# Kernel optimization log

Hardware: AMD Instinct MI355X
Metric: run time of the kernel (lower is better)

The kernel has to match this reference:

```python
import jax, jax.numpy as jnp
import numpy as np
from jax import lax

B, T, L, H, K, NL, NB = 32, 512, 2048, 512, 3, 2, 256
PAD = (K - 1) // 2
EPS = 1e-5


def _predictor_params(key):
    k1, k2 = jax.random.split(key)
    s = 1.0 / np.sqrt(H * K).astype(np.float32)
    return dict(
        conv_w=jax.random.normal(k1, (NL, H, H, K), jnp.float32) * s,
        conv_b=jnp.zeros((NL, H), jnp.float32),
        ln_g=jnp.ones((NL, H), jnp.float32),
        ln_b=jnp.zeros((NL, H), jnp.float32),
        lin_w=jax.random.normal(k2, (H, 1), jnp.float32) * 0.02,
        lin_b=jnp.zeros((1,), jnp.float32),
    )


def setup_inputs():
    key = jax.random.key(0)
    ks = jax.random.split(key, 8)
    inp = {
        'x': jax.random.normal(ks[0], (B, T, H), jnp.float32),
        'src_mask': jnp.zeros((B, T), bool),
        'duration_target': jax.random.randint(ks[1], (B, T), 0, 8, jnp.int32),
        'pitch_target': jax.random.normal(ks[2], (B, T), jnp.float32),
        'energy_target': jax.random.uniform(ks[3], (B, T), jnp.float32),
        'max_len': L,
    }
    for name, k in zip(('dur', 'pit', 'en'), ks[4:7]):
        for p, v in _predictor_params(k).items():
            inp[name + '_' + p] = v
    inp['pitch_bins'] = jnp.linspace(-3.0, 3.0, NB - 1)
    inp['energy_bins'] = jnp.linspace(0.0, 1.0, NB - 1)
    k1, k2 = jax.random.split(ks[7])
    inp['pitch_emb'] = jax.random.normal(k1, (NB, H), jnp.float32) * 0.02
    inp['energy_emb'] = jax.random.normal(k2, (NB, H), jnp.float32) * 0.02
    return inp


def _layer_norm(h, g, b):
    m = jnp.mean(h, -1, keepdims=True)
    v = jnp.var(h, -1, keepdims=True)
    return (h - m) * lax.rsqrt(v + EPS) * g + b


def _predictor(x, cw, cb, lg, lb, lw, lbias, mask):
    # stack of [Conv1d(k=3,same) -> ReLU -> LayerNorm] x NL, then Linear -> 1
    out = x
    for i in range(NL):
        h = lax.conv_general_dilated(out.transpose(0, 2, 1), cw[i], (1,), [(PAD, PAD)],
                                     dimension_numbers=('NCH', 'OIH', 'NCH'))
        h = h.transpose(0, 2, 1) + cb[i]  # [B, T, H]
        out = _layer_norm(jax.nn.relu(h), lg[i], lb[i])
    out = (out @ lw)[..., 0] + lbias[0]  # [B, T]
    return jnp.where(mask, 0.0, out)


def _length_regulate(x, duration, max_len):
    # vectorized equivalent of the per-token expand+concat+pad loop
    csum = jnp.cumsum(duration, axis=1)                     # [B, T]
    frames = jnp.arange(max_len)                            # [L]
    idx = jax.vmap(lambda c: jnp.searchsorted(c, frames, side='right'))(csum)  # [B, L]
    idx = jnp.clip(idx, 0, x.shape[1] - 1)
    out = jnp.take_along_axis(x, idx[:, :, None], axis=1)   # [B, L, H]
    mel_len = jnp.minimum(csum[:, -1], max_len)             # [B]
    out = out * (frames[None, :] < mel_len[:, None])[..., None]
    return out, mel_len


def reference(x, src_mask, duration_target, pitch_target, energy_target, max_len,
              dur_conv_w, dur_conv_b, dur_ln_g, dur_ln_b, dur_lin_w, dur_lin_b,
              pit_conv_w, pit_conv_b, pit_ln_g, pit_ln_b, pit_lin_w, pit_lin_b,
              en_conv_w, en_conv_b, en_ln_g, en_ln_b, en_lin_w, en_lin_b,
              pitch_bins, energy_bins, pitch_emb, energy_emb):
    log_d = _predictor(x, dur_conv_w, dur_conv_b, dur_ln_g, dur_ln_b, dur_lin_w, dur_lin_b, src_mask)
    pitch_pred = _predictor(x, pit_conv_w, pit_conv_b, pit_ln_g, pit_ln_b, pit_lin_w, pit_lin_b, src_mask)
    energy_pred = _predictor(x, en_conv_w, en_conv_b, en_ln_g, en_ln_b, en_lin_w, en_lin_b, src_mask)
    # torch.bucketize(target, bins) (right=False) == searchsorted side='left'
    p_emb = pitch_emb[jnp.searchsorted(pitch_bins, pitch_target, side='left')]
    e_emb = energy_emb[jnp.searchsorted(energy_bins, energy_target, side='left')]
    x2 = x + p_emb + e_emb
    out, mel_len = _length_regulate(x2, duration_target, max_len)
    return (out, pitch_pred, energy_pred, log_d, mel_len)
```

## Files before the change

### kernel.cpp

```cpp
#include <hip/hip_runtime.h>
#include <hip/hip_bf16.h>

#define B_ 32
#define T_ 512
#define TP_ 514
#define L_ 2048
#define H_ 512
#define NRR (B_*T_)
#define KC_ 1536
#define NB_ 256
#define EPS_ 1e-5f
#define XPE ((size_t)B_ * TP_ * H_)

typedef __bf16 bf16;
typedef __bf16 bf16x8 __attribute__((ext_vector_type(8)));
typedef float f32x4 __attribute__((ext_vector_type(4)));

static const size_t WC_BYTES  = (size_t)6 * H_ * KC_ * 2;
static const size_t XP_BYTES  = XPE * 2;
static const size_t Y_BYTES   = (size_t)3 * NRR * H_ * 2;

__device__ __forceinline__ void gload16(const void* g, void* l) {
    __builtin_amdgcn_global_load_lds(
        (const __attribute__((address_space(1))) unsigned int*)g,
        (__attribute__((address_space(3))) unsigned int*)l, 16, 0, 0);
}

__global__ void k_prep_wc(const float* __restrict__ wd, const float* __restrict__ wp,
                          const float* __restrict__ we, bf16* __restrict__ wc) {
    int e = blockIdx.x * 256 + threadIdx.x;
    if (e >= 6 * H_ * KC_) return;
    int m   = e / (H_ * KC_);
    int rem = e % (H_ * KC_);
    int o  = rem / KC_;
    int r2 = rem % KC_;
    int k  = r2 / H_;
    int c  = r2 % H_;
    int p = m >> 1, i = m & 1;
    const float* w = (p == 0) ? wd : (p == 1 ? wp : we);
    float v = w[((size_t)i * H_ * H_ + (size_t)o * H_ + c) * 3 + k];
    wc[e] = (bf16)v;
}

__global__ void k_pad(const float* __restrict__ x, bf16* __restrict__ xp0,
                      bf16* __restrict__ xp1) {
    int wid = threadIdx.x >> 6, lane = threadIdx.x & 63;
    int row = blockIdx.x * 4 + wid;
    int b = row / TP_, tp = row % TP_;
    bf16* d0 = xp0 + (size_t)row * H_ + lane * 8;
    if (tp == 0 || tp == TP_ - 1) {
        bf16x8 z;
#pragma unroll
        for (int i = 0; i < 8; ++i) z[i] = (bf16)0.0f;
        *(bf16x8*)d0 = z;
#pragma unroll
        for (int p = 0; p < 3; ++p)
            *(bf16x8*)(xp1 + p * XPE + (size_t)row * H_ + lane * 8) = z;
    } else {
        const f32x4* p = (const f32x4*)(x + ((size_t)(b * T_ + tp - 1)) * H_ + lane * 8);
        f32x4 u = p[0], v = p[1];
        bf16x8 o;
        o[0] = (bf16)u[0]; o[1] = (bf16)u[1]; o[2] = (bf16)u[2]; o[3] = (bf16)u[3];
        o[4] = (bf16)v[0]; o[5] = (bf16)v[1]; o[6] = (bf16)v[2]; o[7] = (bf16)v[3];
        *(bf16x8*)d0 = o;
    }
}

__global__ void k_scan(const int* __restrict__ dur, int* __restrict__ csum,
                       float* __restrict__ mel_out) {
    int b = blockIdx.x, t = threadIdx.x;
    __shared__ int s[T_];
    s[t] = dur[b * T_ + t];
    __syncthreads();
    for (int off = 1; off < T_; off <<= 1) {
        int v = (t >= off) ? s[t - off] : 0;
        __syncthreads();
        s[t] += v;
        __syncthreads();
    }
    csum[b * T_ + t] = s[t];
    if (t == T_ - 1) mel_out[b] = (float)((s[t] < L_) ? s[t] : L_);
}

__global__ void k_gather(const float* __restrict__ x, const float* __restrict__ pemb,
                         const float* __restrict__ eemb, const float* __restrict__ pt,
                         const float* __restrict__ et, const float* __restrict__ pbins,
                         const float* __restrict__ ebins, const int* __restrict__ csum,
                         float* __restrict__ out) {
    int bi = blockIdx.x;
    int b  = bi >> 9;
    int l0 = (bi & 511) << 2;
    __shared__ int cs[T_];
    __shared__ float pb[NB_ - 1], eb[NB_ - 1];
    cs[threadIdx.x]       = csum[b * T_ + threadIdx.x];
    cs[threadIdx.x + 256] = csum[b * T_ + threadIdx.x + 256];
    if (threadIdx.x < NB_ - 1) {
        pb[threadIdx.x] = pbins[threadIdx.x];
        eb[threadIdx.x] = ebins[threadIdx.x];
    }
    __syncthreads();
    int wid = threadIdx.x >> 6, lane = threadIdx.x & 63;
    int l = l0 + wid;
    int mel = cs[T_ - 1]; if (mel > L_) mel = L_;
    float* op = out + ((size_t)(b * L_ + l)) * H_ + lane * 8;
    if (l >= mel) {
        f32x4 z = {0.f, 0.f, 0.f, 0.f};
        ((f32x4*)op)[0] = z;
        ((f32x4*)op)[1] = z;
        return;
    }
    int lo = 0, hi = T_;
    while (lo < hi) { int mid = (lo + hi) >> 1; if (cs[mid] <= l) lo = mid + 1; else hi = mid; }
    int idx = (lo < T_ - 1) ? lo : (T_ - 1);
    int rr = b * T_ + idx;
    float pv = pt[rr], ev = et[rr];
    int pi, ei;
    { int a = 0, c = NB_ - 1; while (a < c) { int mid = (a + c) >> 1; if (pb[mid] < pv) a = mid + 1; else c = mid; } pi = a; }
    { int a = 0, c = NB_ - 1; while (a < c) { int mid = (a + c) >> 1; if (eb[mid] < ev) a = mid + 1; else c = mid; } ei = a; }
    const f32x4* xp = (const f32x4*)(x    + (size_t)rr * H_ + lane * 8);
    const f32x4* pp = (const f32x4*)(pemb + (size_t)pi * H_ + lane * 8);
    const f32x4* ep = (const f32x4*)(eemb + (size_t)ei * H_ + lane * 8);
    ((f32x4*)op)[0] = xp[0] + pp[0] + ep[0];
    ((f32x4*)op)[1] = xp[1] + pp[1] + ep[1];
}

template<int LAYER>
__global__ __launch_bounds__(512)
void k_gemm(const bf16* __restrict__ Xp, const bf16* __restrict__ Wall,
            const float* __restrict__ cb0, const float* __restrict__ cb1,
            const float* __restrict__ cb2, bf16* __restrict__ Y) {
    __shared__ bf16 lA[128 * 64];
    __shared__ bf16 lB[256 * 64];

    int bid = blockIdx.x;
    int swz = (bid & 7) * 96 + (bid >> 3);
    int rowblk = swz / 6, colblk = swz % 6;
    int p  = colblk >> 1;
    int oB = (colblk & 1) * 256;
    int rowBase = rowblk * 128;

    const bf16* A = (LAYER == 0) ? Xp : (Xp + (size_t)p * XPE);
    const bf16* W = Wall + ((size_t)(2 * p + LAYER) * H_ + oB) * KC_;
    const float* cbp  = (p == 0) ? cb0 : (p == 1 ? cb1 : cb2);
    const float* bias = cbp + LAYER * H_;

    int tid = threadIdx.x;
    int wid = tid >> 6, lane = tid & 63;
    int wr = wid >> 2, wc = wid & 3;
    int lr = lane & 15, kq = lane >> 4;
    int xr = lr & 7;
    int rsub = lane >> 3;
    int csw  = ((lane & 7) ^ rsub) << 3;
    int b = rowBase >> 9, t0 = rowBase & (T_ - 1);

    f32x4 acc[4][4];
#pragma unroll
    for (int m = 0; m < 4; ++m)
#pragma unroll
        for (int n = 0; n < 4; ++n) acc[m][n] = (f32x4){0.f, 0.f, 0.f, 0.f};

    for (int step = 0; step < 24; ++step) {
        int k  = step >> 3;
        int c0 = (step & 7) << 6;
        const bf16* srcA = A + ((size_t)(b * TP_ + t0 + k)) * H_ + c0;
        const bf16* srcB = W + step * 64;
#pragma unroll
        for (int q = 0; q < 2; ++q) {
            int r0 = (wid * 2 + q) * 8;
            gload16(srcA + (size_t)(r0 + rsub) * H_ + csw, lA + r0 * 64);
        }
#pragma unroll
        for (int q = 0; q < 4; ++q) {
            int r0 = (wid * 4 + q) * 8;
            gload16(srcB + (size_t)(r0 + rsub) * KC_ + csw, lB + r0 * 64);
        }
        __syncthreads();
#pragma unroll
        for (int kk = 0; kk < 64; kk += 32) {
            int co = ((((kk >> 3) + kq) ^ xr)) << 3;
            bf16x8 af[4], bfr[4];
#pragma unroll
            for (int m = 0; m < 4; ++m)
                af[m] = *(const bf16x8*)&lA[(wr * 64 + m * 16 + lr) * 64 + co];
#pragma unroll
            for (int n = 0; n < 4; ++n)
                bfr[n] = *(const bf16x8*)&lB[(wc * 64 + n * 16 + lr) * 64 + co];
#pragma unroll
            for (int m = 0; m < 4; ++m)
#pragma unroll
                for (int n = 0; n < 4; ++n)
                    acc[m][n] = __builtin_amdgcn_mfma_f32_16x16x32_bf16(af[m], bfr[n], acc[m][n], 0, 0, 0);
        }
        __syncthreads();
    }

#pragma unroll
    for (int n = 0; n < 4; ++n) {
        int o = oB + wc * 64 + n * 16 + lr;
        float bi = bias[o];
#pragma unroll
        for (int m = 0; m < 4; ++m) {
            int row = rowBase + wr * 64 + m * 16 + 4 * kq;
#pragma unroll
            for (int r = 0; r < 4; ++r)
                Y[((size_t)p * NRR + row + r) * H_ + o] = (bf16)fmaxf(acc[m][n][r] + bi, 0.f);
        }
    }
}

__global__ void k_ln_store(const bf16* __restrict__ Yin,
                           const float* __restrict__ g0, const float* __restrict__ g1,
                           const float* __restrict__ g2,
                           const float* __restrict__ bb0, const float* __restrict__ bb1,
                           const float* __restrict__ bb2, bf16* __restrict__ xp1) {
    int wid = threadIdx.x >> 6, lane = threadIdx.x & 63;
    int rg = blockIdx.x * 4 + wid;
    int p = rg >> 14, r = rg & (NRR - 1);
    const float* g   = (p == 0) ? g0 : (p == 1 ? g1 : g2);
    const float* bta = (p == 0) ? bb0 : (p == 1 ? bb1 : bb2);
    bf16x8 a = *(const bf16x8*)(Yin + ((size_t)p * NRR + r) * H_ + lane * 8);
    float f[8];
#pragma unroll
    for (int i = 0; i < 8; ++i) f[i] = (float)a[i];
    float s1 = 0.f, s2 = 0.f;
#pragma unroll
    for (int i = 0; i < 8; ++i) { s1 += f[i]; s2 += f[i] * f[i]; }
    for (int m = 1; m < 64; m <<= 1) { s1 += __shfl_xor(s1, m); s2 += __shfl_xor(s2, m); }
    float mean = s1 * (1.f / H_);
    float var  = s2 * (1.f / H_) - mean * mean;
    float rs   = rsqrtf(var + EPS_);
    const f32x4* gp = (const f32x4*)g;
    const f32x4* bp = (const f32x4*)bta;
    f32x4 ga = gp[lane * 2], gb = gp[lane * 2 + 1];
    f32x4 ba = bp[lane * 2], bbv = bp[lane * 2 + 1];
    bf16x8 o;
    o[0] = (bf16)((f[0] - mean) * rs * ga[0] + ba[0]);
    o[1] = (bf16)((f[1] - mean) * rs * ga[1] + ba[1]);
    o[2] = (bf16)((f[2] - mean) * rs * ga[2] + ba[2]);
    o[3] = (bf16)((f[3] - mean) * rs * ga[3] + ba[3]);
    o[4] = (bf16)((f[4] - mean) * rs * gb[0] + bbv[0]);
    o[5] = (bf16)((f[5] - mean) * rs * gb[1] + bbv[1]);
    o[6] = (bf16)((f[6] - mean) * rs * gb[2] + bbv[2]);
    o[7] = (bf16)((f[7] - mean) * rs * gb[3] + bbv[3]);
    int bb = r >> 9, t = r & (T_ - 1);
    *(bf16x8*)(xp1 + (size_t)p * XPE + ((size_t)(bb * TP_ + t + 1)) * H_ + lane * 8) = o;
}

__global__ void k_ln_linear(const bf16* __restrict__ Yin,
                            const float* __restrict__ g0, const float* __restrict__ g1,
                            const float* __restrict__ g2,
                            const float* __restrict__ bb0, const float* __restrict__ bb1,
                            const float* __restrict__ bb2,
                            const float* __restrict__ w0p, const float* __restrict__ w1p,
                            const float* __restrict__ w2p,
                            const float* __restrict__ lb0, const float* __restrict__ lb1,
                            const float* __restrict__ lb2,
                            const unsigned char* __restrict__ mask,
                            float* __restrict__ o0, float* __restrict__ o1,
                            float* __restrict__ o2) {
    int wid = threadIdx.x >> 6, lane = threadIdx.x & 63;
    int rg = blockIdx.x * 4 + wid;
    int p = rg >> 14, r = rg & (NRR - 1);
    const float* g   = ((p == 0) ? g0 : (p == 1 ? g1 : g2)) + H_;
    const float* bta = ((p == 0) ? bb0 : (p == 1 ? bb1 : bb2)) + H_;
    const float* lw  = (p == 0) ? w0p : (p == 1 ? w1p : w2p);
    const float* lb  = (p == 0) ? lb0 : (p == 1 ? lb1 : lb2);
    float*       op  = (p == 0) ? o0 : (p == 1 ? o1 : o2);
    bf16x8 a = *(const bf16x8*)(Yin + ((size_t)p * NRR + r) * H_ + lane * 8);
    float f[8];
#pragma unroll
    for (int i = 0; i < 8; ++i) f[i] = (float)a[i];
    float s1 = 0.f, s2 = 0.f;
#pragma unroll
    for (int i = 0; i < 8; ++i) { s1 += f[i]; s2 += f[i] * f[i]; }
    for (int m = 1; m < 64; m <<= 1) { s1 += __shfl_xor(s1, m); s2 += __shfl_xor(s2, m); }
    float mean = s1 * (1.f / H_);
    float var  = s2 * (1.f / H_) - mean * mean;
    float rs   = rsqrtf(var + EPS_);
    const f32x4* gp = (const f32x4*)g;
    const f32x4* bp = (const f32x4*)bta;
    const f32x4* wp = (const f32x4*)lw;
    f32x4 ga = gp[lane * 2], gb = gp[lane * 2 + 1];
    f32x4 ba = bp[lane * 2], bbv = bp[lane * 2 + 1];
    f32x4 wa = wp[lane * 2], wb = wp[lane * 2 + 1];
    float s = ((f[0] - mean) * rs * ga[0] + ba[0]) * wa[0]
            + ((f[1] - mean) * rs * ga[1] + ba[1]) * wa[1]
            + ((f[2] - mean) * rs * ga[2] + ba[2]) * wa[2]
            + ((f[3] - mean) * rs * ga[3] + ba[3]) * wa[3]
            + ((f[4] - mean) * rs * gb[0] + bbv[0]) * wb[0]
            + ((f[5] - mean) * rs * gb[1] + bbv[1]) * wb[1]
            + ((f[6] - mean) * rs * gb[2] + bbv[2]) * wb[2]
            + ((f[7] - mean) * rs * gb[3] + bbv[3]) * wb[3];
    for (int m = 1; m < 64; m <<= 1) s += __shfl_xor(s, m);
    if (lane == 0) op[r] = mask[r] ? 0.f : (s + lb[0]);
}

extern "C" void kernel_launch(void* const* d_in, const int* in_sizes, int n_in,
                              void* d_out, int out_size, void* d_ws, size_t ws_size,
                              hipStream_t stream) {
    const float* x  = (const float*)d_in[0];
    const unsigned char* mask = (const unsigned char*)d_in[1];
    const int*   dur = (const int*)d_in[2];
    const float* pt  = (const float*)d_in[3];
    const float* et  = (const float*)d_in[4];
    const float* cw[3]    = {(const float*)d_in[6],  (const float*)d_in[12], (const float*)d_in[18]};
    const float* cb[3]    = {(const float*)d_in[7],  (const float*)d_in[13], (const float*)d_in[19]};
    const float* lg[3]    = {(const float*)d_in[8],  (const float*)d_in[14], (const float*)d_in[20]};
    const float* lbn[3]   = {(const float*)d_in[9],  (const float*)d_in[15], (const float*)d_in[21]};
    const float* lw[3]    = {(const float*)d_in[10], (const float*)d_in[16], (const float*)d_in[22]};
    const float* lbias[3] = {(const float*)d_in[11], (const float*)d_in[17], (const float*)d_in[23]};
    const float* pbins = (const float*)d_in[24];
    const float* ebins = (const float*)d_in[25];
    const float* pemb  = (const float*)d_in[26];
    const float* eemb  = (const float*)d_in[27];

    float* out0 = (float*)d_out;
    const size_t OUT0 = (size_t)B_ * L_ * H_;
    float* pitch_out  = out0 + OUT0;
    float* energy_out = pitch_out + NRR;
    float* logd_out   = energy_out + NRR;
    float* mel_out    = logd_out + NRR;

    char* ws = (char*)d_ws;
    bf16*  wc   = (bf16*)ws;
    bf16*  xp0  = (bf16*)(ws + WC_BYTES);
    bf16*  xp1  = (bf16*)(ws + WC_BYTES + XP_BYTES);
    bf16*  y    = (bf16*)(ws + WC_BYTES + 4 * XP_BYTES);
    int*   csum = (int*)(ws + WC_BYTES + 4 * XP_BYTES + Y_BYTES);

    k_prep_wc<<<(6 * H_ * KC_ + 255) / 256, 256, 0, stream>>>(cw[0], cw[1], cw[2], wc);
    k_pad<<<B_ * TP_ / 4, 256, 0, stream>>>(x, xp0, xp1);
    k_scan<<<B_, T_, 0, stream>>>(dur, csum, mel_out);
    k_gather<<<B_ * L_ / 4, 256, 0, stream>>>(x, pemb, eemb, pt, et, pbins, ebins, csum, out0);

    k_gemm<0><<<768, 512, 0, stream>>>(xp0, wc, cb[0], cb[1], cb[2], y);
    k_ln_store<<<3 * NRR / 4, 256, 0, stream>>>(y, lg[0], lg[1], lg[2],
                                                lbn[0], lbn[1], lbn[2], xp1);
    k_gemm<1><<<768, 512, 0, stream>>>(xp1, wc, cb[0], cb[1], cb[2], y);
    k_ln_linear<<<3 * NRR / 4, 256, 0, stream>>>(y, lg[0], lg[1], lg[2],
                                                 lbn[0], lbn[1], lbn[2],
                                                 lw[0], lw[1], lw[2],
                                                 lbias[0], lbias[1], lbias[2],
                                                 mask, logd_out, pitch_out, energy_out);
}
```

Before: 274.0 us.

## Rewrite conv GEMM as 256x256 tile with double-buffered LDS and interleaved prefetch

The conv-as-GEMM kernel moves from a 128x256 tile with a single LDS buffer and two barriers per k-step to a 256x256 tile with two LDS buffers of 64 KB each. Global-to-LDS loads for the next k-tiles are issued between quarter-tile MFMA groups, with explicit vmcnt waits, sched barriers and setprio, so memory traffic overlaps compute. The grid halves to 384 blocks. The larger tile doubles reuse of each loaded operand, but it raises register and LDS pressure, which may limit occupancy, and there are fewer blocks to spread across CUs.

```diff
diff --git a/kernel.cpp b/kernel.cpp
--- a/kernel.cpp
+++ b/kernel.cpp
@@ -25,6 +25,10 @@
         (const __attribute__((address_space(1))) unsigned int*)g,
         (__attribute__((address_space(3))) unsigned int*)l, 16, 0, 0);
 }
+
+#define SB() __builtin_amdgcn_sched_barrier(0)
+#define BAR() do { SB(); asm volatile("" ::: "memory"); __builtin_amdgcn_s_barrier(); SB(); } while(0)
+#define VMCNT(N) do { asm volatile("s_waitcnt vmcnt(" #N ")" ::: "memory"); SB(); } while(0)
 
 __global__ void k_prep_wc(const float* __restrict__ wd, const float* __restrict__ wp,
                           const float* __restrict__ we, bf16* __restrict__ wc) {
@@ -125,19 +129,18 @@
 }
 
 template<int LAYER>
-__global__ __launch_bounds__(512)
+__global__ __launch_bounds__(512, 2)
 void k_gemm(const bf16* __restrict__ Xp, const bf16* __restrict__ Wall,
             const float* __restrict__ cb0, const float* __restrict__ cb1,
             const float* __restrict__ cb2, bf16* __restrict__ Y) {
-    __shared__ bf16 lA[128 * 64];
-    __shared__ bf16 lB[256 * 64];
+    __shared__ bf16 lds[65536];
 
     int bid = blockIdx.x;
-    int swz = (bid & 7) * 96 + (bid >> 3);
+    int swz = (bid & 7) * 48 + (bid >> 3);
     int rowblk = swz / 6, colblk = swz % 6;
     int p  = colblk >> 1;
     int oB = (colblk & 1) * 256;
-    int rowBase = rowblk * 128;
+    int rowBase = rowblk * 256;
 
     const bf16* A = (LAYER == 0) ? Xp : (Xp + (size_t)p * XPE);
     const bf16* W = Wall + ((size_t)(2 * p + LAYER) * H_ + oB) * KC_;
@@ -146,66 +149,109 @@
 
     int tid = threadIdx.x;
     int wid = tid >> 6, lane = tid & 63;
-    int wr = wid >> 2, wc = wid & 3;
-    int lr = lane & 15, kq = lane >> 4;
-    int xr = lr & 7;
-    int rsub = lane >> 3;
-    int csw  = ((lane & 7) ^ rsub) << 3;
+    int wm = wid >> 2, wn = wid & 3;
+    int lr = lane & 15, kq = lane >> 4, xk = lr & 7;
+    int srow8 = lane >> 3;
+    int csw = ((lane & 7) ^ srow8) << 3;
     int b = rowBase >> 9, t0 = rowBase & (T_ - 1);
-
-    f32x4 acc[4][4];
-#pragma unroll
-    for (int m = 0; m < 4; ++m)
-#pragma unroll
-        for (int n = 0; n < 4; ++n) acc[m][n] = (f32x4){0.f, 0.f, 0.f, 0.f};
-
-    for (int step = 0; step < 24; ++step) {
-        int k  = step >> 3;
-        int c0 = (step & 7) << 6;
-        const bf16* srcA = A + ((size_t)(b * TP_ + t0 + k)) * H_ + c0;
-        const bf16* srcB = W + step * 64;
-#pragma unroll
-        for (int q = 0; q < 2; ++q) {
-            int r0 = (wid * 2 + q) * 8;
-            gload16(srcA + (size_t)(r0 + rsub) * H_ + csw, lA + r0 * 64);
+    const bf16* Abase = A + ((size_t)(b * TP_ + t0)) * H_;
+
+    f32x4 acc00[4][2], acc01[4][2], acc10[4][2], acc11[4][2];
+#pragma unroll
+    for (int i = 0; i < 4; ++i)
+#pragma unroll
+        for (int j = 0; j < 2; ++j) {
+            acc00[i][j] = (f32x4){0.f,0.f,0.f,0.f}; acc01[i][j] = (f32x4){0.f,0.f,0.f,0.f};
+            acc10[i][j] = (f32x4){0.f,0.f,0.f,0.f}; acc11[i][j] = (f32x4){0.f,0.f,0.f,0.f};
         }
-#pragma unroll
-        for (int q = 0; q < 4; ++q) {
-            int r0 = (wid * 4 + q) * 8;
-            gload16(srcB + (size_t)(r0 + rsub) * KC_ + csw, lB + r0 * 64);
-        }
-        __syncthreads();
-#pragma unroll
-        for (int kk = 0; kk < 64; kk += 32) {
-            int co = ((((kk >> 3) + kq) ^ xr)) << 3;
-            bf16x8 af[4], bfr[4];
-#pragma unroll
-            for (int m = 0; m < 4; ++m)
-                af[m] = *(const bf16x8*)&lA[(wr * 64 + m * 16 + lr) * 64 + co];
-#pragma unroll
-            for (int n = 0; n < 4; ++n)
-                bfr[n] = *(const bf16x8*)&lB[(wc * 64 + n * 16 + lr) * 64 + co];
-#pragma unroll
-            for (int m = 0; m < 4; ++m)
-#pragma unroll
-                for (int n = 0; n < 4; ++n)
-                    acc[m][n] = __builtin_amdgcn_mfma_f32_16x16x32_bf16(af[m], bfr[n], acc[m][n], 0, 0, 0);
-        }
-        __syncthreads();
-    }
-
-#pragma unroll
-    for (int n = 0; n < 4; ++n) {
-        int o = oB + wc * 64 + n * 16 + lr;
-        float bi = bias[o];
-#pragma unroll
-        for (int m = 0; m < 4; ++m) {
-            int row = rowBase + wr * 64 + m * 16 + 4 * kq;
-#pragma unroll
-            for (int r = 0; r < 4; ++r)
-                Y[((size_t)p * NRR + row + r) * H_ + o] = (bf16)fmaxf(acc[m][n][r] + bi, 0.f);
-        }
-    }
+    bf16x8 afr[4][2], bfr[2][2][2];
+
+#define STAGE_A(TAU, MH, D) do { \
+    int k_ = (TAU) >> 3; int c0_ = ((TAU) & 7) << 6; \
+    const bf16* s_ = Abase + ((size_t)(k_ + (MH)*128 + wid*8 + srow8)) * H_ + c0_ + csw; \
+    gload16(s_,                   &lds[(D)*32768 + (MH)*8192 + wid*512]); \
+    gload16(s_ + (size_t)64 * H_, &lds[(D)*32768 + (MH)*8192 + 4096 + wid*512]); \
+} while (0)
+
+#define STAGE_B(TAU, NH, D) do { \
+    const bf16* s_ = W + ((size_t)((NH)*128 + wid*8 + srow8)) * KC_ + (TAU)*64 + csw; \
+    gload16(s_,                    &lds[(D)*32768 + 16384 + (NH)*8192 + wid*512]); \
+    gload16(s_ + (size_t)64 * KC_, &lds[(D)*32768 + 16384 + (NH)*8192 + 4096 + wid*512]); \
+} while (0)
+
+#define LOAD_A(MH, D) do { \
+    _Pragma("unroll") for (int i_ = 0; i_ < 4; ++i_) \
+    _Pragma("unroll") for (int kk_ = 0; kk_ < 2; ++kk_) \
+        afr[i_][kk_] = *(const bf16x8*)&lds[(D)*32768 + (MH)*8192 + \
+            ((wm*4 + i_)*16 + lr)*64 + (((kk_*4 + kq) ^ xk) << 3)]; \
+} while (0)
+
+#define LOAD_B(NH, D) do { \
+    _Pragma("unroll") for (int j_ = 0; j_ < 2; ++j_) \
+    _Pragma("unroll") for (int kk_ = 0; kk_ < 2; ++kk_) \
+        bfr[NH][j_][kk_] = *(const bf16x8*)&lds[(D)*32768 + 16384 + (NH)*8192 + \
+            ((wn*2 + j_)*16 + lr)*64 + (((kk_*4 + kq) ^ xk) << 3)]; \
+} while (0)
+
+#define MFMA_Q(ACC, NH) do { \
+    __builtin_amdgcn_s_setprio(1); \
+    _Pragma("unroll") for (int i_ = 0; i_ < 4; ++i_) \
+    _Pragma("unroll") for (int j_ = 0; j_ < 2; ++j_) \
+    _Pragma("unroll") for (int kk_ = 0; kk_ < 2; ++kk_) \
+        ACC[i_][j_] = __builtin_amdgcn_mfma_f32_16x16x32_bf16(afr[i_][kk_], bfr[NH][j_][kk_], ACC[i_][j_], 0, 0, 0); \
+    __builtin_amdgcn_s_setprio(0); \
+} while (0)
+
+#define KTILE(TAU, D, S1, S2, S3, S4, VMA) do { \
+    LOAD_A(0, D); LOAD_B(0, D); S1; BAR(); MFMA_Q(acc00, 0); BAR(); \
+    LOAD_B(1, D);               S2; BAR(); MFMA_Q(acc01, 1); BAR(); \
+    LOAD_A(1, D);               S3; BAR(); MFMA_Q(acc10, 0); BAR(); \
+                                S4; BAR(); MFMA_Q(acc11, 1); VMA; BAR(); \
+} while (0)
+
+    STAGE_A(0, 0, 0); STAGE_B(0, 0, 0); STAGE_B(0, 1, 0); STAGE_A(0, 1, 0);
+    STAGE_A(1, 0, 1); STAGE_B(1, 0, 1); STAGE_B(1, 1, 1);
+    VMCNT(6);
+    BAR();
+
+#pragma unroll 1
+    for (int it = 0; it < 11; ++it) {
+        int ta = 2 * it, tb = 2 * it + 1;
+        KTILE(ta, 0, STAGE_A(ta + 1, 1, 1), STAGE_A(ta + 2, 0, 0),
+                     STAGE_B(ta + 2, 0, 0), STAGE_B(ta + 2, 1, 0), VMCNT(6));
+        KTILE(tb, 1, STAGE_A(tb + 1, 1, 0), STAGE_A(tb + 2, 0, 1),
+                     STAGE_B(tb + 2, 0, 1), STAGE_B(tb + 2, 1, 1), VMCNT(6));
+    }
+    KTILE(22, 0, STAGE_A(23, 1, 1), (void)0, (void)0, (void)0, VMCNT(0));
+    KTILE(23, 1, (void)0, (void)0, (void)0, (void)0, (void)0);
+
+    float bc[2][2];
+#pragma unroll
+    for (int nh = 0; nh < 2; ++nh)
+#pragma unroll
+        for (int j = 0; j < 2; ++j)
+            bc[nh][j] = bias[oB + nh * 128 + (wn * 2 + j) * 16 + lr];
+
+#define STORE_Q(ACC, MH, NH) do { \
+    _Pragma("unroll") for (int i_ = 0; i_ < 4; ++i_) \
+    _Pragma("unroll") for (int j_ = 0; j_ < 2; ++j_) { \
+        int col_ = oB + (NH)*128 + (wn*2 + j_)*16 + lr; \
+        _Pragma("unroll") for (int r_ = 0; r_ < 4; ++r_) { \
+            int row_ = rowBase + (MH)*128 + (wm*4 + i_)*16 + kq*4 + r_; \
+            Y[((size_t)p * NRR + row_) * H_ + col_] = (bf16)fmaxf(ACC[i_][j_][r_] + bc[NH][j_], 0.f); \
+        } } \
+} while (0)
+
+    STORE_Q(acc00, 0, 0); STORE_Q(acc01, 0, 1);
+    STORE_Q(acc10, 1, 0); STORE_Q(acc11, 1, 1);
+
+#undef STAGE_A
+#undef STAGE_B
+#undef LOAD_A
+#undef LOAD_B
+#undef MFMA_Q
+#undef KTILE
+#undef STORE_Q
 }
 
 __global__ void k_ln_store(const bf16* __restrict__ Yin,
@@ -333,10 +379,10 @@
     k_scan<<<B_, T_, 0, stream>>>(dur, csum, mel_out);
     k_gather<<<B_ * L_ / 4, 256, 0, stream>>>(x, pemb, eemb, pt, et, pbins, ebins, csum, out0);
 
-    k_gemm<0><<<768, 512, 0, stream>>>(xp0, wc, cb[0], cb[1], cb[2], y);
+    k_gemm<0><<<384, 512, 0, stream>>>(xp0, wc, cb[0], cb[1], cb[2], y);
     k_ln_store<<<3 * NRR / 4, 256, 0, stream>>>(y, lg[0], lg[1], lg[2],
                                                 lbn[0], lbn[1], lbn[2], xp1);
-    k_gemm<1><<<768, 512, 0, stream>>>(xp1, wc, cb[0], cb[1], cb[2], y);
+    k_gemm<1><<<384, 512, 0, stream>>>(xp1, wc, cb[0], cb[1], cb[2], y);
     k_ln_linear<<<3 * NRR / 4, 256, 0, stream>>>(y, lg[0], lg[1], lg[2],
                                                  lbn[0], lbn[1], lbn[2],
                                                  lw[0], lw[1], lw[2],
```

Measured after the change: 280.0 us. 2.2% more time.

## Reuse shifted activation tile across conv taps in implicit-GEMM kernel

Applied to the files above, without the earlier changes.

The conv GEMM now loads one 136-row activation tile per 64-channel chunk and reuses it for all three taps by reading shifted rows from LDS, instead of reloading the A tile for each tap. Tiles shrink to 128x128 with 256-thread blocks and twice as many blocks. The block-to-tile mapping is changed so rows are grouped per XCD. This cuts global and LDS traffic for A and halves the number of barrier pairs, at the cost of a larger B tile in LDS per step and a smaller N tile, which lowers B reuse.

```diff
diff --git a/kernel.cpp b/kernel.cpp
--- a/kernel.cpp
+++ b/kernel.cpp
@@ -125,18 +125,19 @@
 }
 
 template<int LAYER>
-__global__ __launch_bounds__(512)
+__global__ __launch_bounds__(256)
 void k_gemm(const bf16* __restrict__ Xp, const bf16* __restrict__ Wall,
             const float* __restrict__ cb0, const float* __restrict__ cb1,
             const float* __restrict__ cb2, bf16* __restrict__ Y) {
-    __shared__ bf16 lA[128 * 64];
-    __shared__ bf16 lB[256 * 64];
+    __shared__ bf16 lA[136 * 64];
+    __shared__ bf16 lB[3 * 128 * 64];
 
     int bid = blockIdx.x;
-    int swz = (bid & 7) * 96 + (bid >> 3);
-    int rowblk = swz / 6, colblk = swz % 6;
-    int p  = colblk >> 1;
-    int oB = (colblk & 1) * 256;
+    int xcd = bid & 7, idx = bid >> 3;
+    int colblk = idx >> 4;
+    int rowblk = xcd * 16 + (idx & 15);
+    int p  = colblk >> 2;
+    int oB = (colblk & 3) * 128;
     int rowBase = rowblk * 128;
 
     const bf16* A = (LAYER == 0) ? Xp : (Xp + (size_t)p * XPE);
@@ -146,12 +147,12 @@
 
     int tid = threadIdx.x;
     int wid = tid >> 6, lane = tid & 63;
-    int wr = wid >> 2, wc = wid & 3;
+    int wm = wid >> 1, wn = wid & 1;
     int lr = lane & 15, kq = lane >> 4;
-    int xr = lr & 7;
     int rsub = lane >> 3;
     int csw  = ((lane & 7) ^ rsub) << 3;
     int b = rowBase >> 9, t0 = rowBase & (T_ - 1);
+    const bf16* Abase = A + ((size_t)(b * TP_ + t0)) * H_;
 
     f32x4 acc[4][4];
 #pragma unroll
@@ -159,48 +160,59 @@
 #pragma unroll
         for (int n = 0; n < 4; ++n) acc[m][n] = (f32x4){0.f, 0.f, 0.f, 0.f};
 
-    for (int step = 0; step < 24; ++step) {
-        int k  = step >> 3;
-        int c0 = (step & 7) << 6;
-        const bf16* srcA = A + ((size_t)(b * TP_ + t0 + k)) * H_ + c0;
-        const bf16* srcB = W + step * 64;
-#pragma unroll
-        for (int q = 0; q < 2; ++q) {
-            int r0 = (wid * 2 + q) * 8;
-            gload16(srcA + (size_t)(r0 + rsub) * H_ + csw, lA + r0 * 64);
+    for (int s = 0; s < 8; ++s) {
+        int c0 = s * 64;
+#pragma unroll
+        for (int q = 0; q < 5; ++q) {
+            int g = q * 4 + wid;
+            if (g < 17)
+                gload16(Abase + (size_t)(g * 8 + rsub) * H_ + c0 + csw, &lA[g * 8 * 64]);
         }
 #pragma unroll
-        for (int q = 0; q < 4; ++q) {
-            int r0 = (wid * 4 + q) * 8;
-            gload16(srcB + (size_t)(r0 + rsub) * KC_ + csw, lB + r0 * 64);
+        for (int tap = 0; tap < 3; ++tap)
+#pragma unroll
+            for (int q = 0; q < 4; ++q) {
+                int g = q * 4 + wid;
+                gload16(W + (size_t)(g * 8 + rsub) * KC_ + tap * H_ + c0 + csw,
+                        &lB[(tap * 128 + g * 8) * 64]);
+            }
+        __syncthreads();
+
+#pragma unroll
+        for (int tap = 0; tap < 3; ++tap) {
+            bf16x8 af[4][2], bfr[4][2];
+            int ka = (lr + tap) & 7, kb = lr & 7;
+#pragma unroll
+            for (int m = 0; m < 4; ++m)
+#pragma unroll
+                for (int kk = 0; kk < 2; ++kk)
+                    af[m][kk] = *(const bf16x8*)&lA[(wm * 64 + m * 16 + lr + tap) * 64 +
+                                                    ((((kk * 4 + kq) ^ ka)) << 3)];
+#pragma unroll
+            for (int n = 0; n < 4; ++n)
+#pragma unroll
+                for (int kk = 0; kk < 2; ++kk)
+                    bfr[n][kk] = *(const bf16x8*)&lB[(tap * 128 + wn * 64 + n * 16 + lr) * 64 +
+                                                     ((((kk * 4 + kq) ^ kb)) << 3)];
+#pragma unroll
+            for (int m = 0; m < 4; ++m)
+#pragma unroll
+                for (int n = 0; n < 4; ++n)
+#pragma unroll
+                    for (int kk = 0; kk < 2; ++kk)
+                        acc[m][n] = __builtin_amdgcn_mfma_f32_16x16x32_bf16(
+                            af[m][kk], bfr[n][kk], acc[m][n], 0, 0, 0);
         }
         __syncthreads();
-#pragma unroll
-        for (int kk = 0; kk < 64; kk += 32) {
-            int co = ((((kk >> 3) + kq) ^ xr)) << 3;
-            bf16x8 af[4], bfr[4];
-#pragma unroll
-            for (int m = 0; m < 4; ++m)
-                af[m] = *(const bf16x8*)&lA[(wr * 64 + m * 16 + lr) * 64 + co];
-#pragma unroll
-            for (int n = 0; n < 4; ++n)
-                bfr[n] = *(const bf16x8*)&lB[(wc * 64 + n * 16 + lr) * 64 + co];
-#pragma unroll
-            for (int m = 0; m < 4; ++m)
-#pragma unroll
-                for (int n = 0; n < 4; ++n)
-                    acc[m][n] = __builtin_amdgcn_mfma_f32_16x16x32_bf16(af[m], bfr[n], acc[m][n], 0, 0, 0);
-        }
-        __syncthreads();
     }
 
 #pragma unroll
     for (int n = 0; n < 4; ++n) {
-        int o = oB + wc * 64 + n * 16 + lr;
+        int o = oB + wn * 64 + n * 16 + lr;
         float bi = bias[o];
 #pragma unroll
         for (int m = 0; m < 4; ++m) {
-            int row = rowBase + wr * 64 + m * 16 + 4 * kq;
+            int row = rowBase + wm * 64 + m * 16 + 4 * kq;
 #pragma unroll
             for (int r = 0; r < 4; ++r)
                 Y[((size_t)p * NRR + row + r) * H_ + o] = (bf16)fmaxf(acc[m][n][r] + bi, 0.f);
@@ -333,10 +345,10 @@
     k_scan<<<B_, T_, 0, stream>>>(dur, csum, mel_out);
     k_gather<<<B_ * L_ / 4, 256, 0, stream>>>(x, pemb, eemb, pt, et, pbins, ebins, csum, out0);
 
-    k_gemm<0><<<768, 512, 0, stream>>>(xp0, wc, cb[0], cb[1], cb[2], y);
+    k_gemm<0><<<1536, 256, 0, stream>>>(xp0, wc, cb[0], cb[1], cb[2], y);
     k_ln_store<<<3 * NRR / 4, 256, 0, stream>>>(y, lg[0], lg[1], lg[2],
                                                 lbn[0], lbn[1], lbn[2], xp1);
-    k_gemm<1><<<768, 512, 0, stream>>>(xp1, wc, cb[0], cb[1], cb[2], y);
+    k_gemm<1><<<1536, 256, 0, stream>>>(xp1, wc, cb[0], cb[1], cb[2], y);
     k_ln_linear<<<3 * NRR / 4, 256, 0, stream>>>(y, lg[0], lg[1], lg[2],
                                                  lbn[0], lbn[1], lbn[2],
                                                  lw[0], lw[1], lw[2],
```

Result: faster. 246.1 us (median of 3 runs) (-10.2%).
